# Kernel optimization log

Hardware: AMD Instinct MI355X
Metric: run time of the kernel (lower is better)

## Reference

```python
import jax, jax.numpy as jnp
import numpy as np
from jax import lax

# Dimensions
B, CIN, COUT = 8, 3, 3
NF = 128          # num_features
K = 9             # DISCO kernel_shape (number of filter basis functions)
HLAT, WLON = 181, 360   # in_shape == out_shape (1-degree equiangular sphere grid)
KH, KW = 5, 5     # compact lat/lon support of each DISCO basis function


def setup_inputs() -> dict:
    key = jax.random.key(0)
    ks = jax.random.split(key, 10)
    s = lambda fan: 1.0 / np.sqrt(fan)
    return {
        "x": jax.random.normal(ks[0], (B, CIN, HLAT, WLON), jnp.float32),
        # DISCO conv: latitude-dependent basis filters, quadrature weights, channel mix
        "psi": jax.random.normal(ks[1], (K, HLAT, KH, KW), jnp.float32) * s(KH * KW),
        "quad": jnp.abs(jax.random.normal(ks[2], (HLAT,), jnp.float32)) * (1.0 / HLAT)
                + jnp.sin(jnp.pi * (jnp.arange(HLAT) + 0.5) / HLAT) * (1.0 / HLAT),
        "w1": jax.random.normal(ks[3], (NF, CIN, K), jnp.float32) * s(CIN * K),
        "b1": jnp.zeros((NF,), jnp.float32),
        # standard conv2d stages
        "w2": jax.random.normal(ks[4], (NF // 2, NF, 5, 5), jnp.float32) * s(NF * 25),
        "b2": jnp.zeros((NF // 2,), jnp.float32),
        "w3": jax.random.normal(ks[5], (COUT, NF // 2, 5, 5), jnp.float32) * s(NF // 2 * 25),
        "b3": jnp.zeros((COUT,), jnp.float32),
    }


def _disco_conv_s2(x, psi, quad, w, b):
    """Discrete-continuous spherical conv: latitude-dependent gather + weighted sum.
    x: [B,C,H,W]; psi: [K,H,KH,KW]; quad: [H]; w: [O,C,K]; b: [O] -> [B,O,H,W]"""
    H, W = x.shape[-2], x.shape[-1]
    rh, rw = KH // 2, KW // 2
    xw = x * quad[None, None, :, None]                       # quadrature-weighted input
    # neighborhood indices: clipped in latitude, circular in longitude
    hi = jnp.clip(jnp.arange(H)[:, None] + jnp.arange(KH)[None, :] - rh, 0, H - 1)  # [H,KH]
    wi = (jnp.arange(W)[:, None] + jnp.arange(KW)[None, :] - rw) % W                # [W,KW]
    g = xw[:, :, hi, :]                                      # [B,C,H,KH,W]
    patches = g[:, :, :, :, wi]                              # [B,C,H,KH,W,KW]
    # project onto latitude-dependent filter basis, then mix channels per basis
    z = jnp.einsum('khij,bchiwj->bckhw', psi, patches)       # [B,C,K,H,W]
    return jnp.einsum('ock,bckhw->bohw', w, z) + b[None, :, None, None]


def _conv2d(x, w, b, pad):
    y = lax.conv_general_dilated(x, w, (1, 1), [(pad, pad), (pad, pad)],
                                 dimension_numbers=('NCHW', 'OIHW', 'NCHW'))
    return y + b[None, :, None, None]


def reference(x, psi, quad, w1, b1, w2, b2, w3, b3):
    h = jax.nn.relu(_disco_conv_s2(x, psi, quad, w1, b1))
    h = jax.nn.relu(_conv2d(h, w2, b2, 2))
    return _conv2d(h, w3, b3, 2)
```

## Files before the change

kernel.cpp:

```cpp
#include <hip/hip_runtime.h>
#include <hip/hip_bf16.h>

#define HLAT 181
#define WLON 360
#define HW (HLAT * WLON)
#define HPAD 188
#define WPAD 368
#define PCH ((size_t)HPAD * WPAD * 16)
#define W2P 372
#define PLANE2 ((size_t)HPAD * W2P * 64)

typedef __attribute__((ext_vector_type(4)))  short short4v;
typedef __attribute__((ext_vector_type(8)))  short short8v;
typedef __attribute__((ext_vector_type(4)))  float f32x4;
typedef __attribute__((ext_vector_type(16))) float f32x16;

static __device__ __forceinline__ ushort bf16_hi_bits(float f) {
  union { float f; unsigned u; } c; c.f = f;
  unsigned u = c.u;
  unsigned rounded = u + 0x7FFF + ((u >> 16) & 1);
  return (ushort)(rounded >> 16);
}
static __device__ __forceinline__ float bf16_to_f(ushort b) {
  union { unsigned u; float f; } c; c.u = ((unsigned)b) << 16;
  return c.f;
}

__global__ __launch_bounds__(256) void k_tw(const float* __restrict__ w2,
                                            const float* __restrict__ w3,
                                            const float* __restrict__ w1,
                                            const float* __restrict__ b1,
                                            ushort* __restrict__ w2f,
                                            ushort* __restrict__ w1f,
                                            ushort* __restrict__ w3f) {
  int idx = blockIdx.x * 256 + threadIdx.x;
  if (idx < 51200) {
    int l   = idx & 63;
    int p   = (idx >> 6) & 1;
    int m   = (idx >> 7) & 1;
    int ch  = (idx >> 8) & 7;
    int tap = idx >> 11;
    int oc  = m * 32 + (l & 31);
    int ci0 = ch * 16 + (l >> 5) * 8;
#pragma unroll
    for (int j = 0; j < 8; ++j) {
      float f = w2[(oc * 128 + ci0 + j) * 25 + tap];
      ushort hi = bf16_hi_bits(f);
      w2f[(size_t)idx * 8 + j] = (p == 0) ? hi : bf16_hi_bits(f - bf16_to_f(hi));
    }
  }
  if (idx < 1024) {
    int l = idx & 63;
    int e = idx >> 6;
    int p  = e & 1;
    int kc = (e >> 1) & 1;
    int m  = e >> 2;
    int oc = m * 32 + (l & 31);
    int k0 = kc * 16 + (l >> 5) * 8;
#pragma unroll
    for (int j = 0; j < 8; ++j) {
      int k = k0 + j;
      float f = (k < 27) ? w1[oc * 27 + k] : (k == 27 ? b1[oc] : 0.f);
      ushort hi = bf16_hi_bits(f);
      w1f[(size_t)idx * 8 + j] = (p == 0) ? hi : bf16_hi_bits(f - bf16_to_f(hi));
    }
  }
  if (idx < 6400) {
    int l   = idx & 63;
    int p   = (idx >> 6) & 1;
    int kc  = (idx >> 7) & 1;
    int tap = idx >> 8;
    int oc  = l & 15;
    int ci0 = kc * 32 + (l >> 4) * 8;
#pragma unroll
    for (int j = 0; j < 8; ++j) {
      float f = (oc < 3) ? w3[(oc * 64 + ci0 + j) * 25 + tap] : 0.f;
      ushort hi = bf16_hi_bits(f);
      w3f[(size_t)idx * 8 + j] = (p == 0) ? hi : bf16_hi_bits(f - bf16_to_f(hi));
    }
  }
}

__global__ __launch_bounds__(256) void k_zring(ushort* __restrict__ h1s) {
  const int i = blockIdx.x * 256 + threadIdx.x;
  if (i >= 4024) return;
  int row, col;
  if (i < 736)       { row = i / 368;              col = i % 368; }
  else if (i < 2576) { int p = i - 736;  row = 183 + p / 368; col = p % 368; }
  else if (i < 2938) { int p = i - 2576; row = 2 + p % 181;   col = p / 181; }
  else               { int p = i - 2938; row = 2 + p % 181;   col = 362 + p / 181; }
  short8v z = {0, 0, 0, 0, 0, 0, 0, 0};
  short8v* d = (short8v*)(h1s + (size_t)blockIdx.y * PCH + ((size_t)row * 368 + col) * 16);
  d[0] = z; d[1] = z;
}

__global__ __launch_bounds__(256) void k_zring2(ushort* __restrict__ h2p) {
  const int i = blockIdx.x * 256 + threadIdx.x;
  if (i >= 4776) return;
  int row, col;
  if (i < 744)       { row = i / W2P;             col = i % W2P; }
  else if (i < 2604) { int p = i - 744;  row = 183 + p / W2P; col = p % W2P; }
  else               { int p = i - 2604; row = 2 + p % 181;
                       int cI = p / 181; col = (cI < 2) ? cI : 360 + cI; }
  short8v z = {0, 0, 0, 0, 0, 0, 0, 0};
  short8v* d = (short8v*)(h2p + (size_t)blockIdx.y * PLANE2 + ((size_t)row * W2P + col) * 64);
#pragma unroll
  for (int k = 0; k < 8; ++k) d[k] = z;
}

__global__ __launch_bounds__(256, 2) void k_l1(const float* __restrict__ x,
    const float* __restrict__ psi, const float* __restrict__ quad,
    const ushort* __restrict__ w1f, ushort* __restrict__ h1s, int b0) {
  const int h = blockIdx.x;
  const int bi = blockIdx.y;
  const int b = b0 + bi;
  const int tid = threadIdx.x;
  __shared__ ushort zl[2][2][368][20];

  if (tid < 180) {
    float z[2][28];
#pragma unroll
    for (int q = 0; q < 28; ++q) { z[0][q] = 0.f; z[1][q] = 0.f; }
#pragma unroll 1
    for (int i = 0; i < 5; ++i) {
      int hi = h + i - 2;
      hi = hi < 0 ? 0 : (hi >= HLAT ? HLAT - 1 : hi);
      const float qv = quad[hi];
      float pv[45];
#pragma unroll
      for (int kk = 0; kk < 9; ++kk)
#pragma unroll
        for (int j = 0; j < 5; ++j)
          pv[kk * 5 + j] = psi[((size_t)(kk * HLAT + h)) * 25 + i * 5 + j];
#pragma unroll
      for (int c = 0; c < 3; ++c) {
        const float* row = x + ((size_t)(b * 3 + c) * HLAT + hi) * WLON;
        float v0[5], v1[5];
#pragma unroll
        for (int j = 0; j < 5; ++j) {
          int wj0 = tid + j - 2; wj0 = wj0 < 0 ? wj0 + WLON : wj0;
          int wj1 = tid + 180 + j - 2; wj1 = wj1 >= WLON ? wj1 - WLON : wj1;
          v0[j] = row[wj0] * qv;
          v1[j] = row[wj1] * qv;
        }
#pragma unroll
        for (int kk = 0; kk < 9; ++kk) {
          float a0 = 0.f, a1 = 0.f;
#pragma unroll
          for (int j = 0; j < 5; ++j) {
            const float p = pv[kk * 5 + j];
            a0 += p * v0[j];
            a1 += p * v1[j];
          }
          z[0][c * 9 + kk] += a0;
          z[1][c * 9 + kk] += a1;
        }
      }
    }
#pragma unroll
    for (int pp = 0; pp < 2; ++pp) {
      const int px = tid + pp * 180;
      z[pp][27] = 1.0f;
      ushort hiv[32], lov[32];
#pragma unroll
      for (int q = 0; q < 28; ++q) {
        const ushort hb = bf16_hi_bits(z[pp][q]);
        hiv[q] = hb;
        lov[q] = bf16_hi_bits(z[pp][q] - bf16_to_f(hb));
      }
#pragma unroll
      for (int q = 28; q < 32; ++q) { hiv[q] = 0; lov[q] = 0; }
#pragma unroll
      for (int kc = 0; kc < 2; ++kc) {
        union { ushort u[8]; short8v v; } ha, hbv, la, lb;
#pragma unroll
        for (int j = 0; j < 8; ++j) {
          ha.u[j] = hiv[kc * 16 + j];     hbv.u[j] = hiv[kc * 16 + 8 + j];
          la.u[j] = lov[kc * 16 + j];     lb.u[j]  = lov[kc * 16 + 8 + j];
        }
        *(short8v*)&zl[0][kc][px][0] = ha.v;
        *(short8v*)&zl[0][kc][px][8] = hbv.v;
        *(short8v*)&zl[1][kc][px][0] = la.v;
        *(short8v*)&zl[1][kc][px][8] = lb.v;
      }
    }
  } else {
    const int t2 = tid - 180;
    if (t2 < 32) {
      const int part = (t2 >> 4) & 1;
      const int kc = (t2 >> 3) & 1;
      const int px = 360 + (t2 & 7);
#pragma unroll
      for (int q = 0; q < 20; ++q) zl[part][kc][px][q] = 0;
    }
  }
  __syncthreads();

  const int wv = tid >> 6;
  const int l = tid & 63;
  const int l31 = l & 31;
  const int q = l >> 5;
  const short8v* wf1 = (const short8v*)w1f;
  short8v A[4][2][2];
#pragma unroll
  for (int m = 0; m < 4; ++m)
#pragma unroll
    for (int kc = 0; kc < 2; ++kc)
#pragma unroll
      for (int p = 0; p < 2; ++p)
        A[m][kc][p] = wf1[(size_t)(((m * 2 + kc) * 2 + p) * 64 + l)];

  ushort* base = h1s + (size_t)bi * 16 * PCH;
#pragma unroll
  for (int nn = 0; nn < 3; ++nn) {
    const int n = wv * 3 + nn;
    const int px = n * 32 + l31;
    const short8v bh0 = *(const short8v*)&zl[0][0][px][q * 8];
    const short8v bl0 = *(const short8v*)&zl[1][0][px][q * 8];
    const short8v bh1 = *(const short8v*)&zl[0][1][px][q * 8];
    const short8v bl1 = *(const short8v*)&zl[1][1][px][q * 8];
    const bool ok = px < 360;
    const size_t pixoff = ((size_t)(h + 2) * WPAD + (px + 2)) * 16;
#pragma unroll
    for (int m = 0; m < 4; ++m) {
      f32x16 acc;
#pragma unroll
      for (int e = 0; e < 16; ++e) acc[e] = 0.f;
      acc = __builtin_amdgcn_mfma_f32_32x32x16_bf16(A[m][0][0], bh0, acc, 0, 0, 0);
      acc = __builtin_amdgcn_mfma_f32_32x32x16_bf16(A[m][0][1], bh0, acc, 0, 0, 0);
      acc = __builtin_amdgcn_mfma_f32_32x32x16_bf16(A[m][0][0], bl0, acc, 0, 0, 0);
      acc = __builtin_amdgcn_mfma_f32_32x32x16_bf16(A[m][1][0], bh1, acc, 0, 0, 0);
      acc = __builtin_amdgcn_mfma_f32_32x32x16_bf16(A[m][1][1], bh1, acc, 0, 0, 0);
      acc = __builtin_amdgcn_mfma_f32_32x32x16_bf16(A[m][1][0], bl1, acc, 0, 0, 0);
      if (ok) {
#pragma unroll
        for (int r = 0; r < 4; ++r) {
          const int rb = 8 * r + 4 * q;
          const int ch = m * 2 + (rb >> 4);
          const int ci0 = rb & 15;
          short4v h4, l4;
#pragma unroll
          for (int j = 0; j < 4; ++j) {
            const float v = fmaxf(acc[r * 4 + j], 0.f);
            const ushort hb = bf16_hi_bits(v);
            h4[j] = (short)hb;
            l4[j] = (short)bf16_hi_bits(v - bf16_to_f(hb));
          }
          *(short4v*)(base + (size_t)ch * PCH + pixoff + ci0) = h4;
          *(short4v*)(base + (size_t)(8 + ch) * PCH + pixoff + ci0) = l4;
        }
      }
    }
  }
}

__global__ __launch_bounds__(256, 2) void k_conv2(const ushort* __restrict__ h1s,
    const ushort* __restrict__ w2f, const float* __restrict__ b2,
    ushort* __restrict__ h2p) {
  __shared__ ushort act[2][2][12][40][16];
  const int x0 = blockIdx.x * 32;
  const int y0 = blockIdx.y * 8;
  const int bi = blockIdx.z;
  const int tid = threadIdx.x;
  const int wv = tid >> 6;
  const int m  = wv >> 1;
  const int wr = wv & 1;
  const int l = tid & 63;
  const int l31 = l & 31;
  const int q8 = (l >> 5) * 8;

  f32x16 acc[4];
#pragma unroll
  for (int r = 0; r < 4; ++r)
#pragma unroll
    for (int e = 0; e < 16; ++e) acc[r][e] = 0.f;

  const short8v* wf = (const short8v*)w2f;
  const ushort* pbase = h1s + (size_t)bi * 16 * PCH;

  auto stage = [&](int buf, int ch) {
#pragma unroll
    for (int s = 0; s < 12; ++s) {
      const int k = wv * 12 + s;
      const int part = k / 24;
      const int rem = k - part * 24;
      const int t = rem >> 1;
      const int slot = rem & 1;
      const ushort* pl = pbase + (size_t)(part * 8 + ch) * PCH;
      if (slot == 0) {
        const ushort* g = pl + ((size_t)(y0 + t) * WPAD + (x0 + (l >> 1))) * 16 + (l & 1) * 8;
        __builtin_amdgcn_global_load_lds(
            (const __attribute__((address_space(1))) unsigned int*)g,
            (__attribute__((address_space(3))) unsigned int*)&act[buf][part][t][0][0], 16, 0, 0);
      } else {
        const ushort* g = pl + ((size_t)(y0 + t) * WPAD + (x0 + 32 + (l >> 3))) * 16 + (l & 7) * 2;
        __builtin_amdgcn_global_load_lds(
            (const __attribute__((address_space(1))) unsigned int*)g,
            (__attribute__((address_space(3))) unsigned int*)&act[buf][part][t][32][0], 4, 0, 0);
      }
    }
  };

  stage(0, 0);
  asm volatile("s_waitcnt vmcnt(0)" ::: "memory");
  __syncthreads();

#pragma unroll 1
  for (int ch = 0; ch < 8; ++ch) {
    const int cur = ch & 1;
    if (ch < 7) stage(cur ^ 1, ch + 1);
#pragma unroll 1
    for (int dj = 0; dj < 5; ++dj) {
      short8v aw[5][2];
#pragma unroll
      for (int di = 0; di < 5; ++di) {
        const size_t e0 = (size_t)(((di * 5 + dj) * 8 + ch) * 4 + m * 2) * 64 + l;
        aw[di][0] = wf[e0];
        aw[di][1] = wf[e0 + 64];
      }
      __builtin_amdgcn_s_setprio(1);
#pragma unroll
      for (int rr = 0; rr < 8; ++rr) {
        const int t = wr * 4 + rr;
        const int c = l31 + dj;
        const short8v bh = *(const short8v*)&act[cur][0][t][c][q8];
        const short8v bl = *(const short8v*)&act[cur][1][t][c][q8];
#pragma unroll
        for (int di = 0; di < 5; ++di) {
          const int r = rr - di;
          if (r < 0 || r > 3) continue;
          acc[r] = __builtin_amdgcn_mfma_f32_32x32x16_bf16(aw[di][0], bh, acc[r], 0, 0, 0);
          acc[r] = __builtin_amdgcn_mfma_f32_32x32x16_bf16(aw[di][1], bh, acc[r], 0, 0, 0);
          acc[r] = __builtin_amdgcn_mfma_f32_32x32x16_bf16(aw[di][0], bl, acc[r], 0, 0, 0);
        }
      }
      __builtin_amdgcn_s_setprio(0);
    }
    asm volatile("s_waitcnt vmcnt(0)" ::: "memory");
    __syncthreads();
  }

  const int xg = x0 + l31;
  ushort* hp = h2p + (size_t)bi * 2 * PLANE2;
  if (xg < WLON) {
#pragma unroll
    for (int r = 0; r < 4; ++r) {
      const int y = y0 + wr * 4 + r;
      if (y >= HLAT) continue;
      const size_t po = ((size_t)(y + 2) * W2P + (xg + 2)) * 64;
#pragma unroll
      for (int run = 0; run < 4; ++run) {
        const int oc0 = m * 32 + 8 * run + (q8 >> 1);
        short4v h4, l4;
#pragma unroll
        for (int j = 0; j < 4; ++j) {
          const float v = fmaxf(acc[r][run * 4 + j] + b2[oc0 + j], 0.f);
          const ushort hb = bf16_hi_bits(v);
          h4[j] = (short)hb;
          l4[j] = (short)bf16_hi_bits(v - bf16_to_f(hb));
        }
        *(short4v*)(hp + po + oc0) = h4;
        *(short4v*)(hp + PLANE2 + po + oc0) = l4;
      }
    }
  }
}

__global__ __launch_bounds__(256, 2) void k_conv3(const ushort* __restrict__ h2p,
    const ushort* __restrict__ w3f, const float* __restrict__ b3,
    float* __restrict__ out, int b0) {
  __shared__ ushort act[2][12][20][72];
  const int x0 = blockIdx.x * 16;
  const int y0 = blockIdx.y * 8;
  const int bi = blockIdx.z;
  const int tid = threadIdx.x;
  const int wv = tid >> 6;
  const int l = tid & 63;

  {
    const ushort* pb = h2p + (size_t)bi * 2 * PLANE2;
    float4 v[6][3];
#pragma unroll
    for (int pr = 0; pr < 6; ++pr) {
      const int pair = wv * 6 + pr;
      const int part = pair / 12;
      const int row = pair % 12;
      const ushort* src = pb + (size_t)part * PLANE2 +
                          ((size_t)(y0 + row) * W2P + x0) * 64;
      v[pr][0] = *(const float4*)((const char*)src + l * 16);
      v[pr][1] = *(const float4*)((const char*)src + 1024 + l * 16);
      if (l < 32) v[pr][2] = *(const float4*)((const char*)src + 2048 + l * 16);
    }
#pragma unroll
    for (int pr = 0; pr < 6; ++pr) {
      const int pair = wv * 6 + pr;
      const int part = pair / 12;
      const int row = pair % 12;
#pragma unroll
      for (int k2 = 0; k2 < 3; ++k2) {
        if (k2 == 2 && l >= 32) continue;
        const int B = k2 * 1024 + l * 16;
        const int col = B >> 7;
        const int ci = (B & 127) >> 1;
        *(short8v*)&act[part][row][col][ci] = *(short8v*)&v[pr][k2];
      }
    }
  }
  __syncthreads();

  f32x4 acc[2];
#pragma unroll
  for (int r = 0; r < 2; ++r)
#pragma unroll
    for (int e = 0; e < 4; ++e) acc[r][e] = 0.f;

  const short8v* wf3 = (const short8v*)w3f;
  const int c16 = l & 15;
  const int koff0 = ((l >> 4) & 3) * 8;

#pragma unroll 1
  for (int kc = 0; kc < 2; ++kc) {
#pragma unroll 1
    for (int dj = 0; dj < 5; ++dj) {
      short8v A[5][2];
#pragma unroll
      for (int di = 0; di < 5; ++di) {
        const size_t e0 = (size_t)(((di * 5 + dj) * 2 + kc) * 2) * 64 + l;
        A[di][0] = wf3[e0];
        A[di][1] = wf3[e0 + 64];
      }
      const int c = c16 + dj;
      const int koff = kc * 32 + koff0;
      __builtin_amdgcn_s_setprio(1);
#pragma unroll
      for (int tt = 0; tt < 6; ++tt) {
        const int t = wv * 2 + tt;
        const short8v bh = *(const short8v*)&act[0][t][c][koff];
        const short8v bl = *(const short8v*)&act[1][t][c][koff];
#pragma unroll
        for (int di = 0; di < 5; ++di) {
          const int r = tt - di;
          if (r < 0 || r > 1) continue;
          acc[r] = __builtin_amdgcn_mfma_f32_16x16x32_bf16(A[di][0], bh, acc[r], 0, 0, 0);
          acc[r] = __builtin_amdgcn_mfma_f32_16x16x32_bf16(A[di][1], bh, acc[r], 0, 0, 0);
          acc[r] = __builtin_amdgcn_mfma_f32_16x16x32_bf16(A[di][0], bl, acc[r], 0, 0, 0);
        }
      }
      __builtin_amdgcn_s_setprio(0);
    }
  }

  const int px = x0 + c16;
  const int b = b0 + bi;
  if ((l >> 4) == 0 && px < WLON) {
    const float bb[3] = {b3[0], b3[1], b3[2]};
#pragma unroll
    for (int r = 0; r < 2; ++r) {
      const int y = y0 + wv * 2 + r;
      if (y >= HLAT) continue;
#pragma unroll
      for (int j = 0; j < 3; ++j)
        out[((size_t)(b * 3 + j) * HLAT + y) * WLON + px] = acc[r][j] + bb[j];
    }
  }
}

extern "C" void kernel_launch(void* const* d_in, const int* in_sizes, int n_in,
                              void* d_out, int out_size, void* d_ws, size_t ws_size,
                              hipStream_t stream) {
  const float* x    = (const float*)d_in[0];
  const float* psi  = (const float*)d_in[1];
  const float* quad = (const float*)d_in[2];
  const float* w1   = (const float*)d_in[3];
  const float* b1   = (const float*)d_in[4];
  const float* w2   = (const float*)d_in[5];
  const float* b2   = (const float*)d_in[6];
  const float* w3   = (const float*)d_in[7];
  const float* b3   = (const float*)d_in[8];
  float* out = (float*)d_out;
  float* ws  = (float*)d_ws;

  ushort* w2f = (ushort*)ws;
  ushort* w1f = (ushort*)(ws + 204800);
  ushort* w3f = (ushort*)(ws + 208896);
  const size_t HEAD = 234496;

  size_t wsf = ws_size / 4;
  const size_t h1s_f = PCH * 8;
  const size_t h2p_f = PLANE2;
  const size_t per_b = h1s_f + h2p_f;
  int bc = 8;
  while (bc > 1 && HEAD + (size_t)bc * per_b > wsf) bc >>= 1;

  ushort* h1s = (ushort*)(ws + HEAD);
  ushort* h2p = (ushort*)(ws + HEAD + (size_t)bc * h1s_f);

  k_tw<<<dim3(200), dim3(256), 0, stream>>>(w2, w3, w1, b1, w2f, w1f, w3f);
  k_zring<<<dim3(16, bc * 16), dim3(256), 0, stream>>>(h1s);
  k_zring2<<<dim3(19, bc * 2), dim3(256), 0, stream>>>(h2p);

  for (int b0 = 0; b0 < 8; b0 += bc) {
    int cur = 8 - b0 < bc ? 8 - b0 : bc;
    k_l1<<<dim3(HLAT, cur), dim3(256), 0, stream>>>(x, psi, quad, w1f, h1s, b0);
    k_conv2<<<dim3(12, 23, cur), dim3(256), 0, stream>>>(h1s, w2f, b2, h2p);
    k_conv3<<<dim3(23, 23, cur), dim3(256), 0, stream>>>(h2p, w3f, b3, out, b0);
  }
}
```

Before: 746.3 us.

## Split DISCO layer into separate basis-projection and MFMA channel-mix kernels

The fused layer-1 kernel, which used 180 threads to compute two pixels each and then ran the MFMA mix from shared memory, is split in two. A new 384-thread kernel computes the 28-wide basis projection for one pixel per thread and writes hi/lo bf16 splits to a global scratch buffer. A second kernel runs the channel-mix MFMA reading that buffer. The scratch buffer aliases the conv2 output buffer, so the ring-zeroing of that buffer moves inside the batch loop after the mix kernel. This raises parallelism in the projection step at the cost of an extra kernel launch and a global-memory round trip.

```diff
diff --git a/kernel.cpp b/kernel.cpp
--- a/kernel.cpp
+++ b/kernel.cpp
@@ -9,6 +9,7 @@
 #define PCH ((size_t)HPAD * WPAD * 16)
 #define W2P 372
 #define PLANE2 ((size_t)HPAD * W2P * 64)
+#define ZROW ((size_t)384 * 64)
 
 typedef __attribute__((ext_vector_type(4)))  short short4v;
 typedef __attribute__((ext_vector_type(8)))  short short8v;
@@ -108,94 +109,83 @@
   for (int k = 0; k < 8; ++k) d[k] = z;
 }
 
-__global__ __launch_bounds__(256, 2) void k_l1(const float* __restrict__ x,
+__global__ __launch_bounds__(384, 2) void k_z(const float* __restrict__ x,
     const float* __restrict__ psi, const float* __restrict__ quad,
-    const ushort* __restrict__ w1f, ushort* __restrict__ h1s, int b0) {
+    ushort* __restrict__ zbuf, int b0) {
   const int h = blockIdx.x;
   const int bi = blockIdx.y;
   const int b = b0 + bi;
   const int tid = threadIdx.x;
-  __shared__ ushort zl[2][2][368][20];
-
-  if (tid < 180) {
-    float z[2][28];
-#pragma unroll
-    for (int q = 0; q < 28; ++q) { z[0][q] = 0.f; z[1][q] = 0.f; }
+  ushort* dst = zbuf + (size_t)(bi * HLAT + h) * ZROW + (size_t)tid * 64;
+  if (tid >= 360) {
+    short8v zz = {0, 0, 0, 0, 0, 0, 0, 0};
+    short8v* d8 = (short8v*)dst;
+#pragma unroll
+    for (int k = 0; k < 8; ++k) d8[k] = zz;
+    return;
+  }
+  float z[28];
+#pragma unroll
+  for (int q = 0; q < 28; ++q) z[q] = 0.f;
 #pragma unroll 1
-    for (int i = 0; i < 5; ++i) {
-      int hi = h + i - 2;
-      hi = hi < 0 ? 0 : (hi >= HLAT ? HLAT - 1 : hi);
-      const float qv = quad[hi];
-      float pv[45];
-#pragma unroll
-      for (int kk = 0; kk < 9; ++kk)
-#pragma unroll
-        for (int j = 0; j < 5; ++j)
-          pv[kk * 5 + j] = psi[((size_t)(kk * HLAT + h)) * 25 + i * 5 + j];
-#pragma unroll
-      for (int c = 0; c < 3; ++c) {
-        const float* row = x + ((size_t)(b * 3 + c) * HLAT + hi) * WLON;
-        float v0[5], v1[5];
-#pragma unroll
-        for (int j = 0; j < 5; ++j) {
-          int wj0 = tid + j - 2; wj0 = wj0 < 0 ? wj0 + WLON : wj0;
-          int wj1 = tid + 180 + j - 2; wj1 = wj1 >= WLON ? wj1 - WLON : wj1;
-          v0[j] = row[wj0] * qv;
-          v1[j] = row[wj1] * qv;
-        }
-#pragma unroll
-        for (int kk = 0; kk < 9; ++kk) {
-          float a0 = 0.f, a1 = 0.f;
-#pragma unroll
-          for (int j = 0; j < 5; ++j) {
-            const float p = pv[kk * 5 + j];
-            a0 += p * v0[j];
-            a1 += p * v1[j];
-          }
-          z[0][c * 9 + kk] += a0;
-          z[1][c * 9 + kk] += a1;
-        }
-      }
-    }
-#pragma unroll
-    for (int pp = 0; pp < 2; ++pp) {
-      const int px = tid + pp * 180;
-      z[pp][27] = 1.0f;
-      ushort hiv[32], lov[32];
-#pragma unroll
-      for (int q = 0; q < 28; ++q) {
-        const ushort hb = bf16_hi_bits(z[pp][q]);
-        hiv[q] = hb;
-        lov[q] = bf16_hi_bits(z[pp][q] - bf16_to_f(hb));
-      }
-#pragma unroll
-      for (int q = 28; q < 32; ++q) { hiv[q] = 0; lov[q] = 0; }
-#pragma unroll
-      for (int kc = 0; kc < 2; ++kc) {
-        union { ushort u[8]; short8v v; } ha, hbv, la, lb;
-#pragma unroll
-        for (int j = 0; j < 8; ++j) {
-          ha.u[j] = hiv[kc * 16 + j];     hbv.u[j] = hiv[kc * 16 + 8 + j];
-          la.u[j] = lov[kc * 16 + j];     lb.u[j]  = lov[kc * 16 + 8 + j];
-        }
-        *(short8v*)&zl[0][kc][px][0] = ha.v;
-        *(short8v*)&zl[0][kc][px][8] = hbv.v;
-        *(short8v*)&zl[1][kc][px][0] = la.v;
-        *(short8v*)&zl[1][kc][px][8] = lb.v;
-      }
-    }
-  } else {
-    const int t2 = tid - 180;
-    if (t2 < 32) {
-      const int part = (t2 >> 4) & 1;
-      const int kc = (t2 >> 3) & 1;
-      const int px = 360 + (t2 & 7);
-#pragma unroll
-      for (int q = 0; q < 20; ++q) zl[part][kc][px][q] = 0;
-    }
-  }
-  __syncthreads();
-
+  for (int i = 0; i < 5; ++i) {
+    int hi = h + i - 2;
+    hi = hi < 0 ? 0 : (hi >= HLAT ? HLAT - 1 : hi);
+    const float qv = quad[hi];
+    float pv[45];
+#pragma unroll
+    for (int kk = 0; kk < 9; ++kk)
+#pragma unroll
+      for (int j = 0; j < 5; ++j)
+        pv[kk * 5 + j] = psi[((size_t)(kk * HLAT + h)) * 25 + i * 5 + j];
+#pragma unroll
+    for (int c = 0; c < 3; ++c) {
+      const float* row = x + ((size_t)(b * 3 + c) * HLAT + hi) * WLON;
+      float v[5];
+#pragma unroll
+      for (int j = 0; j < 5; ++j) {
+        int wj = tid + j - 2;
+        wj = wj < 0 ? wj + WLON : (wj >= WLON ? wj - WLON : wj);
+        v[j] = row[wj] * qv;
+      }
+#pragma unroll
+      for (int kk = 0; kk < 9; ++kk) {
+        float a = 0.f;
+#pragma unroll
+        for (int j = 0; j < 5; ++j) a += pv[kk * 5 + j] * v[j];
+        z[c * 9 + kk] += a;
+      }
+    }
+  }
+  z[27] = 1.0f;
+  ushort hiv[32], lov[32];
+#pragma unroll
+  for (int q = 0; q < 28; ++q) {
+    const ushort hb = bf16_hi_bits(z[q]);
+    hiv[q] = hb;
+    lov[q] = bf16_hi_bits(z[q] - bf16_to_f(hb));
+  }
+#pragma unroll
+  for (int q = 28; q < 32; ++q) { hiv[q] = 0; lov[q] = 0; }
+#pragma unroll
+  for (int part = 0; part < 2; ++part)
+#pragma unroll
+    for (int kc = 0; kc < 2; ++kc)
+#pragma unroll
+      for (int half = 0; half < 2; ++half) {
+        union { ushort u[8]; short8v v8; } t8;
+#pragma unroll
+        for (int j = 0; j < 8; ++j)
+          t8.u[j] = (part == 0 ? hiv : lov)[kc * 16 + half * 8 + j];
+        *(short8v*)&dst[part * 32 + kc * 16 + half * 8] = t8.v8;
+      }
+}
+
+__global__ __launch_bounds__(256, 2) void k_mv(const ushort* __restrict__ zbuf,
+    const ushort* __restrict__ w1f, ushort* __restrict__ h1s) {
+  const int h = blockIdx.x;
+  const int bi = blockIdx.y;
+  const int tid = threadIdx.x;
   const int wv = tid >> 6;
   const int l = tid & 63;
   const int l31 = l & 31;
@@ -211,14 +201,16 @@
         A[m][kc][p] = wf1[(size_t)(((m * 2 + kc) * 2 + p) * 64 + l)];
 
   ushort* base = h1s + (size_t)bi * 16 * PCH;
+  const ushort* zrow = zbuf + (size_t)(bi * HLAT + h) * ZROW;
 #pragma unroll
   for (int nn = 0; nn < 3; ++nn) {
     const int n = wv * 3 + nn;
     const int px = n * 32 + l31;
-    const short8v bh0 = *(const short8v*)&zl[0][0][px][q * 8];
-    const short8v bl0 = *(const short8v*)&zl[1][0][px][q * 8];
-    const short8v bh1 = *(const short8v*)&zl[0][1][px][q * 8];
-    const short8v bl1 = *(const short8v*)&zl[1][1][px][q * 8];
+    const ushort* zp = zrow + (size_t)px * 64 + q * 8;
+    const short8v bh0 = *(const short8v*)(zp + 0);
+    const short8v bh1 = *(const short8v*)(zp + 16);
+    const short8v bl0 = *(const short8v*)(zp + 32);
+    const short8v bl1 = *(const short8v*)(zp + 48);
     const bool ok = px < 360;
     const size_t pixoff = ((size_t)(h + 2) * WPAD + (px + 2)) * 16;
 #pragma unroll
@@ -494,14 +486,16 @@
 
   ushort* h1s = (ushort*)(ws + HEAD);
   ushort* h2p = (ushort*)(ws + HEAD + (size_t)bc * h1s_f);
+  ushort* zbuf = h2p;
 
   k_tw<<<dim3(200), dim3(256), 0, stream>>>(w2, w3, w1, b1, w2f, w1f, w3f);
   k_zring<<<dim3(16, bc * 16), dim3(256), 0, stream>>>(h1s);
-  k_zring2<<<dim3(19, bc * 2), dim3(256), 0, stream>>>(h2p);
 
   for (int b0 = 0; b0 < 8; b0 += bc) {
     int cur = 8 - b0 < bc ? 8 - b0 : bc;
-    k_l1<<<dim3(HLAT, cur), dim3(256), 0, stream>>>(x, psi, quad, w1f, h1s, b0);
+    k_z<<<dim3(HLAT, cur), dim3(384), 0, stream>>>(x, psi, quad, zbuf, b0);
+    k_mv<<<dim3(HLAT, cur), dim3(256), 0, stream>>>(zbuf, w1f, h1s);
+    k_zring2<<<dim3(19, cur * 2), dim3(256), 0, stream>>>(h2p);
     k_conv2<<<dim3(12, 23, cur), dim3(256), 0, stream>>>(h1s, w2f, b2, h2p);
     k_conv3<<<dim3(23, 23, cur), dim3(256), 0, stream>>>(h2p, w3f, b3, out, b0);
   }
```

Result: slower. 768.0 us (+2.9%).
